# Optimization experiments

Measured on AMD Instinct MI355X. Metric: run time of the kernel, lower is better.

Reference implementation:

```python
import math
import jax, jax.numpy as jnp
import numpy as np

B, T, S, C, E = 16, 1024, 1024, 1024, 1024
NORM_C = 0.5


def setup_inputs() -> dict:
    key = jax.random.key(0)
    ks = jax.random.split(key, 9)
    return {
        "x": jax.random.normal(ks[0], (B, T, C), dtype=jnp.float32),
        "target_embedding": jax.random.normal(ks[1], (B, T, E), dtype=jnp.float32),
        "enc_keys": jax.random.normal(ks[2], (B, E, S), dtype=jnp.float32),      # encoder_out[0]
        "enc_values": jax.random.normal(ks[3], (B, S, E), dtype=jnp.float32),    # encoder_out[1]
        "encoder_padding_mask": jax.random.randint(ks[4], (B, S), 0, 2).astype(bool),
        "w_in": jax.random.normal(ks[5], (E, C), dtype=jnp.float32) / np.sqrt(C),
        "b_in": jnp.zeros((E,), dtype=jnp.float32),
        "w_out": jax.random.normal(ks[6], (C, E), dtype=jnp.float32) / np.sqrt(E),
        "b_out": jnp.zeros((C,), dtype=jnp.float32),
    }


def reference(x, target_embedding, enc_keys, enc_values, encoder_padding_mask,
              w_in, b_in, w_out, b_out):
    scale = jnp.float32(math.sqrt(NORM_C))
    residual = x
    # in_projection + target embedding, rescale
    h = (jnp.einsum("btc,ec->bte", x, w_in) + b_in + target_embedding) * scale
    # attention scores: bmm with keys [B,E,S]
    scores = jnp.einsum("bte,bes->bts", h, enc_keys)
    neg_inf = jnp.float32(float("-inf"))
    scores = jnp.where(encoder_padding_mask[:, None, :], neg_inf, scores)
    attn_scores = jax.nn.softmax(scores, axis=-1)
    # weighted sum of values
    ctx = jnp.einsum("bts,bse->bte", attn_scores, enc_values)
    # data-dependent rescale: multiply by sqrt(valid token count)
    s = jnp.float32(S) - jnp.sum(encoder_padding_mask.astype(ctx.dtype), axis=1, keepdims=True)  # [B,1]
    s = s[:, :, None]  # [B,1,1]
    ctx = ctx * (s * jax.lax.rsqrt(s))
    out = (jnp.einsum("bte,ce->btc", ctx, w_out) + b_out + residual) * scale
    return (out, attn_scores)
```

## Files before the change

### kernel.cpp

```cpp
#include <hip/hip_runtime.h>


#define SCALE_F 0.70710678118654752440f

constexpr int BB = 16, TT = 1024, SS = 1024, CC = 1024, EE = 1024;

typedef float    f32x4 __attribute__((ext_vector_type(4)));
typedef _Float16 f16x8 __attribute__((ext_vector_type(8)));
typedef _Float16 f16x4 __attribute__((ext_vector_type(4)));

__device__ __forceinline__ void gload_lds16(const _Float16* g, _Float16* l) {
  __builtin_amdgcn_global_load_lds((const __attribute__((address_space(1))) void*)g,
                                   (__attribute__((address_space(3))) void*)l,
                                   16, 0, 0);
}

__global__ __launch_bounds__(256) void cvt_f16(const float* __restrict__ s,
                                               _Float16* __restrict__ d, long n) {
  long i = ((long)blockIdx.x * 256 + threadIdx.x) * 8;
  if (i >= n) return;
  f32x4 a = *(const f32x4*)(s + i);
  f32x4 b = *(const f32x4*)(s + i + 4);
  f16x8 h;
  h[0]=(_Float16)a[0]; h[1]=(_Float16)a[1]; h[2]=(_Float16)a[2]; h[3]=(_Float16)a[3];
  h[4]=(_Float16)b[0]; h[5]=(_Float16)b[1]; h[6]=(_Float16)b[2]; h[7]=(_Float16)b[3];
  *(f16x8*)(d + i) = h;
}

__global__ __launch_bounds__(256) void transpose_cvt(const float* __restrict__ src,
                                                     _Float16* __restrict__ dst,
                                                     int R, int Cc) {
  __shared__ float tile[64][65];
  const int b = blockIdx.z;
  const int r0 = blockIdx.y * 64, c0 = blockIdx.x * 64;
  const int t = threadIdx.x;
  const int tr = t >> 4, tc4 = (t & 15) * 4;
  const float* s = src + (size_t)b * R * Cc;
#pragma unroll
  for (int i = 0; i < 4; ++i) {
    f32x4 v = *(const f32x4*)(s + (size_t)(r0 + i * 16 + tr) * Cc + c0 + tc4);
    tile[i * 16 + tr][tc4 + 0] = v[0]; tile[i * 16 + tr][tc4 + 1] = v[1];
    tile[i * 16 + tr][tc4 + 2] = v[2]; tile[i * 16 + tr][tc4 + 3] = v[3];
  }
  __syncthreads();
  _Float16* d = dst + (size_t)b * Cc * R;
#pragma unroll
  for (int j = 0; j < 4; ++j) {
    const int cl = j * 16 + tr;
    f16x4 h;
    h[0] = (_Float16)tile[tc4 + 0][cl]; h[1] = (_Float16)tile[tc4 + 1][cl];
    h[2] = (_Float16)tile[tc4 + 2][cl]; h[3] = (_Float16)tile[tc4 + 3][cl];
    *(f16x4*)(d + (size_t)(c0 + cl) * R + r0 + tc4) = h;
  }
}

__global__ __launch_bounds__(256) void mask_prep(const unsigned char* __restrict__ mraw,
                                                 float* __restrict__ maskneg,
                                                 float* __restrict__ sscale) {
  const int b = blockIdx.x, t = threadIdx.x;
  __shared__ int bytemode_sh, cnt_sh;
  if (t == 0) { bytemode_sh = 0; cnt_sh = 0; }
  __syncthreads();
  const unsigned int* mu = (const unsigned int*)mraw;
  int local = 0;
  for (int i = t; i < (BB * SS) / 4; i += 256) {
    unsigned int v = mu[i];
    if (v != 0u && v != 1u && v != 0x3f800000u) local = 1;
  }
  if (local) atomicOr(&bytemode_sh, 1);
  __syncthreads();
  const int bytemode = bytemode_sh;
  int cnt = 0;
  for (int s = t; s < SS; s += 256) {
    int m = bytemode ? (mraw[b * SS + s] != 0) : (mu[b * SS + s] != 0u);
    maskneg[b * SS + s] = m ? -__builtin_inff() : 0.0f;
    cnt += m;
  }
#pragma unroll
  for (int o = 32; o; o >>= 1) cnt += __shfl_down(cnt, o);
  if ((t & 63) == 0) atomicAdd(&cnt_sh, cnt);
  __syncthreads();
  if (t == 0) {
    float sv = (float)SS - (float)cnt_sh;
    sscale[b] = sv * rsqrtf(sv);
  }
}

template <int EPI>
__global__ __launch_bounds__(256)
void gemm_nt(const _Float16* __restrict__ A, const _Float16* __restrict__ Bmat,
             long aStride, long bStride, long oStride,
             int M, int N, int K,
             void* __restrict__ outp,
             const float* __restrict__ bias,
             const float* __restrict__ addmat,
             const float* __restrict__ extra) {
  constexpr int BM = 128, BN = 128, BK = 64;
  constexpr int EPS = 68;
  __shared__ __attribute__((aligned(16))) _Float16 smem[2][(BM + BN) * BK];

  const int t = threadIdx.x;
  const int lane = t & 63;
  const int wid = t >> 6;
  const int wr = wid >> 1, wc = wid & 1;
  const int z = blockIdx.z;

  const int gy = gridDim.y;
  const int fblk = blockIdx.x + (blockIdx.y << 3);
  const int wg = (fblk & 7) * gy + (fblk >> 3);
  const long rowBase = (long)(wg >> 3) * BM;
  const long colBase = (long)(wg & 7) * BN;

  const _Float16* Ag = A + (size_t)z * aStride + rowBase * K;
  const _Float16* Bg = Bmat + (size_t)z * bStride + colBase * K;

  const int srow = t >> 3;
  const int scol = 8 * ((t & 7) ^ (srow & 7));

  f32x4 acc[4][4] = {};

  const int lo = lane & 15, hi = lane >> 4;
  const int sx = lo & 7;

  auto stage = [&](int buf, int k0) {
    _Float16* As = &smem[buf][0];
    _Float16* Bs = &smem[buf][BM * BK];
#pragma unroll
    for (int q = 0; q < 4; ++q)
      gload_lds16(Ag + (size_t)(q * 32 + srow) * K + k0 + scol, &As[(q * 256 + t) * 8]);
#pragma unroll
    for (int q = 0; q < 4; ++q)
      gload_lds16(Bg + (size_t)(q * 32 + srow) * K + k0 + scol, &Bs[(q * 256 + t) * 8]);
  };

  stage(0, 0);
  asm volatile("s_waitcnt vmcnt(0)" ::: "memory");
  __syncthreads();

  int cur = 0;
  for (int k0 = 0; k0 < K; k0 += BK) {
    if (k0 + BK < K) stage(cur ^ 1, k0 + BK);
    const _Float16* As = &smem[cur][0];
    const _Float16* Bs = &smem[cur][BM * BK];
#pragma unroll
    for (int ks = 0; ks < 2; ++ks) {
      f16x8 a[4], b[4];
#pragma unroll
      for (int m = 0; m < 4; ++m) {
        const int slotA = (ks * 4 + hi) ^ sx;
        a[m] = *(const f16x8*)&As[(wr * 64 + m * 16 + lo) * BK + slotA * 8];
      }
#pragma unroll
      for (int n = 0; n < 4; ++n) {
        const int slotB = (ks * 4 + hi) ^ sx;
        b[n] = *(const f16x8*)&Bs[(wc * 64 + n * 16 + lo) * BK + slotB * 8];
      }
#pragma unroll
      for (int m = 0; m < 4; ++m)
#pragma unroll
        for (int n = 0; n < 4; ++n)
          acc[m][n] = __builtin_amdgcn_mfma_f32_16x16x32_f16(a[m], b[n], acc[m][n], 0, 0, 0);
    }
    __syncthreads();
    cur ^= 1;
  }

  const int fr = lane & 15;
  const int fq = (lane >> 4) * 4;
  const int er = lane >> 2;
  const int ec = (lane & 3) * 16;
  const long gc0 = colBase + wc * 64 + ec;
  float* ep = (float*)&smem[0][0] + wid * (16 * EPS);

  f32x4 biasv[4], maskv[4], av[4];
  float sc = 0.f;
  if constexpr (EPI == 1 || EPI == 4) {
#pragma unroll
    for (int i = 0; i < 4; ++i) biasv[i] = *(const f32x4*)&bias[gc0 + i * 4];
    const long gr0 = rowBase + wr * 64 + er;
#pragma unroll
    for (int i = 0; i < 4; ++i) av[i] = *(const f32x4*)&addmat[gr0 * N + gc0 + i * 4];
  }
  if constexpr (EPI == 2) {
#pragma unroll
    for (int i = 0; i < 4; ++i) maskv[i] = *(const f32x4*)&extra[(size_t)z * N + gc0 + i * 4];
  }
  if constexpr (EPI == 3) sc = extra[z];

#pragma unroll
  for (int m = 0; m < 4; ++m) {
#pragma unroll
    for (int n = 0; n < 4; ++n)
#pragma unroll
      for (int j = 0; j < 4; ++j)
        ep[(fq + j) * EPS + n * 16 + fr] = acc[m][n][j];
    __syncthreads();
    const long gr = rowBase + wr * 64 + m * 16 + er;
    f32x4 r[4];
#pragma unroll
    for (int i = 0; i < 4; ++i) r[i] = *(const f32x4*)&ep[er * EPS + ec + i * 4];
    f32x4 a_cur[4];
    if constexpr (EPI == 1 || EPI == 4) {
#pragma unroll
      for (int i = 0; i < 4; ++i) a_cur[i] = av[i];
      if (m < 3) {
        const long grn = gr + 16;
#pragma unroll
        for (int i = 0; i < 4; ++i) av[i] = *(const f32x4*)&addmat[grn * N + gc0 + i * 4];
      }
    }
    if constexpr (EPI == 1) {
      _Float16* o = (_Float16*)outp + gr * N + gc0;
#pragma unroll
      for (int g = 0; g < 2; ++g) {
        f32x4 v0 = (r[2 * g] + biasv[2 * g] + a_cur[2 * g]) * SCALE_F;
        f32x4 v1 = (r[2 * g + 1] + biasv[2 * g + 1] + a_cur[2 * g + 1]) * SCALE_F;
        f16x8 h;
        h[0]=(_Float16)v0[0]; h[1]=(_Float16)v0[1]; h[2]=(_Float16)v0[2]; h[3]=(_Float16)v0[3];
        h[4]=(_Float16)v1[0]; h[5]=(_Float16)v1[1]; h[6]=(_Float16)v1[2]; h[7]=(_Float16)v1[3];
        *(f16x8*)(o + g * 8) = h;
      }
    } else if constexpr (EPI == 2) {
      float* o = (float*)outp + (size_t)z * oStride + gr * N + gc0;
#pragma unroll
      for (int i = 0; i < 4; ++i) *(f32x4*)(o + i * 4) = r[i] + maskv[i];
    } else if constexpr (EPI == 3) {
      _Float16* o = (_Float16*)outp + (size_t)z * oStride + gr * N + gc0;
#pragma unroll
      for (int g = 0; g < 2; ++g) {
        f32x4 v0 = r[2 * g] * sc;
        f32x4 v1 = r[2 * g + 1] * sc;
        f16x8 h;
        h[0]=(_Float16)v0[0]; h[1]=(_Float16)v0[1]; h[2]=(_Float16)v0[2]; h[3]=(_Float16)v0[3];
        h[4]=(_Float16)v1[0]; h[5]=(_Float16)v1[1]; h[6]=(_Float16)v1[2]; h[7]=(_Float16)v1[3];
        *(f16x8*)(o + g * 8) = h;
      }
    } else {
      float* o = (float*)outp + gr * N + gc0;
#pragma unroll
      for (int i = 0; i < 4; ++i)
        *(f32x4*)(o + i * 4) = (r[i] + biasv[i] + a_cur[i]) * SCALE_F;
    }
    __syncthreads();
  }
}

__global__ __launch_bounds__(256) void softmax_k(float* __restrict__ attn,
                                                 _Float16* __restrict__ attn16) {
  const size_t row = blockIdx.x;
  float* p = attn + row * SS;
  const int t = threadIdx.x;
  f32x4 v = *(const f32x4*)(p + t * 4);
  __shared__ float red[8];
  float m = fmaxf(fmaxf(v[0], v[1]), fmaxf(v[2], v[3]));
#pragma unroll
  for (int o = 32; o; o >>= 1) m = fmaxf(m, __shfl_xor(m, o));
  if (!(t & 63)) red[t >> 6] = m;
  __syncthreads();
  m = fmaxf(fmaxf(red[0], red[1]), fmaxf(red[2], red[3]));
  f32x4 e;
  e[0] = __expf(v[0] - m); e[1] = __expf(v[1] - m);
  e[2] = __expf(v[2] - m); e[3] = __expf(v[3] - m);
  float s = e[0] + e[1] + e[2] + e[3];
#pragma unroll
  for (int o = 32; o; o >>= 1) s += __shfl_xor(s, o);
  if (!(t & 63)) red[4 + (t >> 6)] = s;
  __syncthreads();
  s = red[4] + red[5] + red[6] + red[7];
  const float inv = 1.0f / s;
  f32x4 o4; o4[0]=e[0]*inv; o4[1]=e[1]*inv; o4[2]=e[2]*inv; o4[3]=e[3]*inv;
  *(f32x4*)(p + t * 4) = o4;
  f16x4 h; h[0]=(_Float16)o4[0]; h[1]=(_Float16)o4[1];
  h[2]=(_Float16)o4[2]; h[3]=(_Float16)o4[3];
  *(f16x4*)(attn16 + row * SS + t * 4) = h;
}

extern "C" void kernel_launch(void* const* d_in, const int* in_sizes, int n_in,
                              void* d_out, int out_size, void* d_ws, size_t ws_size,
                              hipStream_t stream) {
  const float* x     = (const float*)d_in[0];
  const float* te    = (const float*)d_in[1];
  const float* keys  = (const float*)d_in[2];
  const float* vals  = (const float*)d_in[3];
  const void*  mask  = d_in[4];
  const float* w_in  = (const float*)d_in[5];
  const float* b_in  = (const float*)d_in[6];
  const float* w_out = (const float*)d_in[7];
  const float* b_out = (const float*)d_in[8];

  char* ws = (char*)d_ws;
  const size_t MB32 = 33554432;
  _Float16* buf0   = (_Float16*)(ws);
  _Float16* buf1   = (_Float16*)(ws + MB32);
  _Float16* keysT  = (_Float16*)(ws + 2 * MB32);
  _Float16* valsT  = (_Float16*)(ws + 3 * MB32);
  _Float16* win16  = (_Float16*)(ws + 4 * MB32);
  _Float16* wout16 = (_Float16*)(ws + 4 * MB32 + 2097152);
  float*    maskneg= (float*)   (ws + 4 * MB32 + 2 * 2097152);
  float*    sscale = (float*)   (ws + 4 * MB32 + 2 * 2097152 + 65536);

  float* out_main = (float*)d_out;
  float* attn_out = (float*)d_out + (size_t)BB * TT * CC;

  cvt_f16<<<dim3(16777216 / 2048), 256, 0, stream>>>(x, buf0, 16777216);
  cvt_f16<<<dim3(1048576 / 2048), 256, 0, stream>>>(w_in, win16, 1048576);
  cvt_f16<<<dim3(1048576 / 2048), 256, 0, stream>>>(w_out, wout16, 1048576);
  transpose_cvt<<<dim3(SS / 64, EE / 64, BB), 256, 0, stream>>>(keys, keysT, EE, SS);
  transpose_cvt<<<dim3(EE / 64, SS / 64, BB), 256, 0, stream>>>(vals, valsT, SS, EE);
  mask_prep<<<dim3(BB), 256, 0, stream>>>((const unsigned char*)mask, maskneg, sscale);

  gemm_nt<1><<<dim3(EE / 128, (BB * TT) / 128, 1), 256, 0, stream>>>(
      buf0, win16, 0, 0, 0, BB * TT, EE, CC, buf1, b_in, te, nullptr);
  gemm_nt<2><<<dim3(SS / 128, TT / 128, BB), 256, 0, stream>>>(
      buf1, keysT, (long)TT * EE, (long)SS * EE, (long)TT * SS,
      TT, SS, EE, attn_out, nullptr, nullptr, maskneg);
  softmax_k<<<dim3(BB * TT), 256, 0, stream>>>(attn_out, buf1);
  gemm_nt<3><<<dim3(EE / 128, TT / 128, BB), 256, 0, stream>>>(
      buf1, valsT, (long)TT * SS, (long)EE * SS, (long)TT * EE,
      TT, EE, SS, buf0, nullptr, nullptr, sscale);
  gemm_nt<4><<<dim3(CC / 128, (BB * TT) / 128, 1), 256, 0, stream>>>(
      buf0, wout16, 0, 0, 0, BB * TT, CC, EE, out_main, b_out, x, nullptr);
}
```

Before: 337.1 us.

## Replace direct global-to-LDS loads with register-staged prefetch pipeline in GEMMs

The GEMM main loop now loads tiles from global memory into registers two steps ahead, writes them to swizzled shared memory after reading the current fragments, and runs the MFMA block at raised wave priority, with one barrier per iteration. This takes the place of the global_load_lds double-buffered scheme, with the aim of hiding global latency behind compute. The change also adds launch bounds for two blocks per CU and generalises the block-index swizzle. In exchange it uses more registers for the staging buffers and adds LDS write traffic.

```diff
diff --git a/kernel.cpp b/kernel.cpp
--- a/kernel.cpp
+++ b/kernel.cpp
@@ -9,11 +9,8 @@
 typedef _Float16 f16x8 __attribute__((ext_vector_type(8)));
 typedef _Float16 f16x4 __attribute__((ext_vector_type(4)));
 
-__device__ __forceinline__ void gload_lds16(const _Float16* g, _Float16* l) {
-  __builtin_amdgcn_global_load_lds((const __attribute__((address_space(1))) void*)g,
-                                   (__attribute__((address_space(3))) void*)l,
-                                   16, 0, 0);
-}
+#define LGKM0()  asm volatile("s_waitcnt lgkmcnt(0)" ::: "memory")
+#define SBAR()   asm volatile("s_barrier" ::: "memory")
 
 __global__ __launch_bounds__(256) void cvt_f16(const float* __restrict__ s,
                                                _Float16* __restrict__ d, long n) {
@@ -87,8 +84,8 @@
 }
 
 template <int EPI>
-__global__ __launch_bounds__(256)
-void gemm_nt(const _Float16* __restrict__ A, const _Float16* __restrict__ Bmat,
+__global__ __launch_bounds__(256, 2)
+void gemm_rs(const _Float16* __restrict__ A, const _Float16* __restrict__ Bmat,
              long aStride, long bStride, long oStride,
              int M, int N, int K,
              void* __restrict__ outp,
@@ -96,7 +93,6 @@
              const float* __restrict__ addmat,
              const float* __restrict__ extra) {
   constexpr int BM = 128, BN = 128, BK = 64;
-  constexpr int EPS = 68;
   __shared__ __attribute__((aligned(16))) _Float16 smem[2][(BM + BN) * BK];
 
   const int t = threadIdx.x;
@@ -104,67 +100,83 @@
   const int wid = t >> 6;
   const int wr = wid >> 1, wc = wid & 1;
   const int z = blockIdx.z;
-
-  const int gy = gridDim.y;
-  const int fblk = blockIdx.x + (blockIdx.y << 3);
-  const int wg = (fblk & 7) * gy + (fblk >> 3);
-  const long rowBase = (long)(wg >> 3) * BM;
-  const long colBase = (long)(wg & 7) * BN;
+  const int lo = lane & 15, hi = lane >> 4;
+  const int sx = lo & 7;
+  const int nt = K >> 6;
+
+  const int gx = gridDim.x;
+  const int fblk = blockIdx.x + blockIdx.y * gx;
+  const int q = (gx * gridDim.y) >> 3;
+  const int wg = (fblk & 7) * q + (fblk >> 3);
+  const long rowBase = (long)(wg / gx) * BM;
+  const long colBase = (long)(wg % gx) * BN;
 
   const _Float16* Ag = A + (size_t)z * aStride + rowBase * K;
   const _Float16* Bg = Bmat + (size_t)z * bStride + colBase * K;
 
-  const int srow = t >> 3;
-  const int scol = 8 * ((t & 7) ^ (srow & 7));
-
+  const int srow = t >> 1;
+  const int sh4 = (t & 1) * 4;
+
+  f16x8 ra[4], rb[4];
   f32x4 acc[4][4] = {};
 
-  const int lo = lane & 15, hi = lane >> 4;
-  const int sx = lo & 7;
-
-  auto stage = [&](int buf, int k0) {
+  auto gload = [&](int u) {
+    const _Float16* ap = Ag + (size_t)srow * K + u * 64 + sh4 * 8;
+    const _Float16* bp = Bg + (size_t)srow * K + u * 64 + sh4 * 8;
+#pragma unroll
+    for (int i = 0; i < 4; ++i) ra[i] = *(const f16x8*)(ap + i * 8);
+#pragma unroll
+    for (int i = 0; i < 4; ++i) rb[i] = *(const f16x8*)(bp + i * 8);
+  };
+  auto swrite = [&](int buf) {
     _Float16* As = &smem[buf][0];
     _Float16* Bs = &smem[buf][BM * BK];
-#pragma unroll
-    for (int q = 0; q < 4; ++q)
-      gload_lds16(Ag + (size_t)(q * 32 + srow) * K + k0 + scol, &As[(q * 256 + t) * 8]);
-#pragma unroll
-    for (int q = 0; q < 4; ++q)
-      gload_lds16(Bg + (size_t)(q * 32 + srow) * K + k0 + scol, &Bs[(q * 256 + t) * 8]);
+    const int rb8 = srow & 7;
+#pragma unroll
+    for (int i = 0; i < 4; ++i)
+      *(f16x8*)&As[srow * 64 + ((sh4 + i) ^ rb8) * 8] = ra[i];
+#pragma unroll
+    for (int i = 0; i < 4; ++i)
+      *(f16x8*)&Bs[srow * 64 + ((sh4 + i) ^ rb8) * 8] = rb[i];
   };
 
-  stage(0, 0);
-  asm volatile("s_waitcnt vmcnt(0)" ::: "memory");
-  __syncthreads();
-
-  int cur = 0;
-  for (int k0 = 0; k0 < K; k0 += BK) {
-    if (k0 + BK < K) stage(cur ^ 1, k0 + BK);
-    const _Float16* As = &smem[cur][0];
-    const _Float16* Bs = &smem[cur][BM * BK];
+  gload(0);
+  swrite(0);
+  gload(1);
+  LGKM0();
+  SBAR();
+
+  for (int u = 0; u < nt; ++u) {
+    const _Float16* As = &smem[u & 1][0];
+    const _Float16* Bs = &smem[u & 1][BM * BK];
+    f16x8 a[2][4], b[2][4];
 #pragma unroll
     for (int ks = 0; ks < 2; ++ks) {
-      f16x8 a[4], b[4];
-#pragma unroll
-      for (int m = 0; m < 4; ++m) {
-        const int slotA = (ks * 4 + hi) ^ sx;
-        a[m] = *(const f16x8*)&As[(wr * 64 + m * 16 + lo) * BK + slotA * 8];
-      }
-#pragma unroll
-      for (int n = 0; n < 4; ++n) {
-        const int slotB = (ks * 4 + hi) ^ sx;
-        b[n] = *(const f16x8*)&Bs[(wc * 64 + n * 16 + lo) * BK + slotB * 8];
-      }
-#pragma unroll
-      for (int m = 0; m < 4; ++m)
-#pragma unroll
-        for (int n = 0; n < 4; ++n)
-          acc[m][n] = __builtin_amdgcn_mfma_f32_16x16x32_f16(a[m], b[n], acc[m][n], 0, 0, 0);
+      const int slot = (ks * 4 + hi) ^ sx;
+#pragma unroll
+      for (int mi = 0; mi < 4; ++mi)
+        a[ks][mi] = *(const f16x8*)&As[(wr * 64 + mi * 16 + lo) * 64 + slot * 8];
+#pragma unroll
+      for (int ni = 0; ni < 4; ++ni)
+        b[ks][ni] = *(const f16x8*)&Bs[(wc * 64 + ni * 16 + lo) * 64 + slot * 8];
     }
-    __syncthreads();
-    cur ^= 1;
-  }
-
+    if (u + 1 < nt) swrite((u + 1) & 1);
+    if (u + 2 < nt) gload(u + 2);
+    __builtin_amdgcn_s_setprio(1);
+#pragma unroll
+    for (int ks = 0; ks < 2; ++ks)
+#pragma unroll
+      for (int mi = 0; mi < 4; ++mi)
+#pragma unroll
+        for (int ni = 0; ni < 4; ++ni)
+          acc[mi][ni] = __builtin_amdgcn_mfma_f32_16x16x32_f16(
+              a[ks][mi], b[ks][ni], acc[mi][ni], 0, 0, 0);
+    __builtin_amdgcn_s_setprio(0);
+    LGKM0();
+    SBAR();
+  }
+
+  constexpr int EPS = 68;
   const int fr = lane & 15;
   const int fq = (lane >> 4) * 4;
   const int er = lane >> 2;
@@ -309,15 +321,15 @@
   transpose_cvt<<<dim3(EE / 64, SS / 64, BB), 256, 0, stream>>>(vals, valsT, SS, EE);
   mask_prep<<<dim3(BB), 256, 0, stream>>>((const unsigned char*)mask, maskneg, sscale);
 
-  gemm_nt<1><<<dim3(EE / 128, (BB * TT) / 128, 1), 256, 0, stream>>>(
+  gemm_rs<1><<<dim3(EE / 128, (BB * TT) / 128, 1), 256, 0, stream>>>(
       buf0, win16, 0, 0, 0, BB * TT, EE, CC, buf1, b_in, te, nullptr);
-  gemm_nt<2><<<dim3(SS / 128, TT / 128, BB), 256, 0, stream>>>(
+  gemm_rs<2><<<dim3(SS / 128, TT / 128, BB), 256, 0, stream>>>(
       buf1, keysT, (long)TT * EE, (long)SS * EE, (long)TT * SS,
       TT, SS, EE, attn_out, nullptr, nullptr, maskneg);
   softmax_k<<<dim3(BB * TT), 256, 0, stream>>>(attn_out, buf1);
-  gemm_nt<3><<<dim3(EE / 128, TT / 128, BB), 256, 0, stream>>>(
+  gemm_rs<3><<<dim3(EE / 128, TT / 128, BB), 256, 0, stream>>>(
       buf1, valsT, (long)TT * SS, (long)EE * SS, (long)TT * EE,
       TT, EE, SS, buf0, nullptr, nullptr, sscale);
-  gemm_nt<4><<<dim3(CC / 128, (BB * TT) / 128, 1), 256, 0, stream>>>(
+  gemm_rs<4><<<dim3(CC / 128, (BB * TT) / 128, 1), 256, 0, stream>>>(
       buf0, wout16, 0, 0, 0, BB * TT, CC, EE, out_main, b_out, x, nullptr);
 }
```

Result: no change. 341.7 us, median of 2 (+1.4%).
